# Optimization experiments

Measured on AMD Instinct MI355X. Metric: run time of the kernel, lower is better.

Reference implementation:

```python
import jax, jax.numpy as jnp
import numpy as np

B, N_AIM, N_DET, C = 4, 2048, 2048, 256  # inplanes=256, inter_channels=128


def _lin(x, w, b):
    # torch nn.Linear: y = x @ W^T + b, weight shape [out, in]
    return jnp.einsum('bnc,dc->bnd', x, w) + b


def setup_inputs() -> dict:
    key = jax.random.key(0)
    ks = jax.random.split(key, 16)
    s = 1.0 / np.sqrt(C)
    inp = {
        'detect': jax.random.normal(ks[0], (B, N_DET, C), jnp.float32),
        'aim': jax.random.normal(ks[1], (B, N_AIM, C), jnp.float32),
    }
    names = ['g', 'g2', 'theta', 'phi', 'W', 'Q']
    for i, nm in enumerate(names):
        inp[nm + '_w'] = jax.random.uniform(ks[2 + 2 * i], (C, C), jnp.float32, -s, s)
        inp[nm + '_b'] = jax.random.uniform(ks[3 + 2 * i], (C,), jnp.float32, -s, s)
    return inp


def reference(detect, aim, g_w, g_b, g2_w, g2_b, theta_w, theta_b, phi_w, phi_b, W_w, W_b, Q_w, Q_b):
    b, na, c = aim.shape
    nd = detect.shape[1]
    ic = c // 2  # inter_channels

    # view(B, ic, -1) on a contiguous [B, N, C] tensor -> row-major reshape to [B, ic, 2N]
    d_x = _lin(detect, g_w, g_b).reshape(b, ic, -1).transpose(0, 2, 1)      # (B, 2Nd, ic)
    a_x = _lin(aim, g2_w, g2_b).reshape(b, ic, -1).transpose(0, 2, 1)       # (B, 2Na, ic)
    theta_x = _lin(aim, theta_w, theta_b).reshape(b, ic, -1).transpose(0, 2, 1)  # (B, 2Na, ic)
    phi_x = _lin(detect, phi_w, phi_b).reshape(b, ic, -1)                   # (B, ic, 2Nd)

    f = jnp.matmul(theta_x, phi_x)                 # (B, 2Na, 2Nd)
    f_div_C = f / f.shape[-1]                      # scale by 2*Nd
    fi_div_C = jnp.swapaxes(f, 1, 2) / f.shape[-2] # (B, 2Nd, 2Na), scale by 2*Na

    non_aim = jnp.matmul(f_div_C, d_x)             # (B, 2Na, ic)
    non_aim = non_aim.transpose(0, 2, 1).reshape(b, na, c)
    non_aim = _lin(non_aim, W_w, W_b) + aim

    non_det = jnp.matmul(fi_div_C, a_x)            # (B, 2Nd, ic)
    non_det = non_det.transpose(0, 2, 1).reshape(b, nd, c)
    non_det = _lin(non_det, Q_w, Q_b) + detect

    return (non_det, non_aim)
```

## Files before the change

kernel.cpp:

```cpp
#include <hip/hip_runtime.h>


typedef __attribute__((ext_vector_type(4))) float  f32x4;
typedef __attribute__((ext_vector_type(8))) __bf16 bf16x8;
typedef __attribute__((ext_vector_type(8))) unsigned short u16x8;
typedef __attribute__((ext_vector_type(4))) unsigned short u16x4;

__device__ inline unsigned short f2bf(float f) {
    union { float f; unsigned u; } c; c.f = f;
    unsigned r = c.u + 0x7FFF + ((c.u >> 16) & 1);
    return (unsigned short)(r >> 16);
}
__device__ inline bf16x8 ldfrag(const unsigned short* p) {
    return __builtin_bit_cast(bf16x8, *(const u16x8*)p);
}

__global__ __launch_bounds__(256)
void lin4_kernel(const float* __restrict__ aim, const float* __restrict__ detect,
                 const float* __restrict__ w_th, const float* __restrict__ b_th,
                 const float* __restrict__ w_g2, const float* __restrict__ b_g2,
                 const float* __restrict__ w_ph, const float* __restrict__ b_ph,
                 const float* __restrict__ w_g,  const float* __restrict__ b_g,
                 unsigned short* __restrict__ T,  unsigned short* __restrict__ Ga,
                 unsigned short* __restrict__ P,  unsigned short* __restrict__ Gd)
{
    const int z = blockIdx.z, set = blockIdx.x;
    const float* A  = z ? detect : aim;
    const float* Wm = z ? (set ? w_g : w_ph) : (set ? w_g2 : w_th);
    const float* Bv = z ? (set ? b_g : b_ph) : (set ? b_g2 : b_th);
    unsigned short* O = z ? (set ? Gd : P) : (set ? Ga : T);
    const int m0 = blockIdx.y * 64;

    __shared__ unsigned short As[64][40];
    __shared__ unsigned short Bs[256][40];

    const int tid = threadIdx.x, lane = tid & 63, w = tid >> 6;
    const int wr = w >> 1, wc = w & 1, q = lane >> 4, ln = lane & 15;

    f32x4 acc[2][8] = {};

    for (int k0 = 0; k0 < 256; k0 += 32) {
        #pragma unroll
        for (int i = 0; i < 2; ++i) {
            int c = tid + i * 256, row = c >> 3, c4 = c & 7;
            float4 v = *((const float4*)(A + (size_t)(m0 + row) * 256 + k0) + c4);
            u16x4 p; p[0]=f2bf(v.x); p[1]=f2bf(v.y); p[2]=f2bf(v.z); p[3]=f2bf(v.w);
            *(u16x4*)&As[row][c4 * 4] = p;
        }
        #pragma unroll
        for (int i = 0; i < 8; ++i) {
            int c = tid + i * 256, row = c >> 3, c4 = c & 7;
            float4 v = *((const float4*)(Wm + (size_t)row * 256 + k0) + c4);
            u16x4 p; p[0]=f2bf(v.x); p[1]=f2bf(v.y); p[2]=f2bf(v.z); p[3]=f2bf(v.w);
            *(u16x4*)&Bs[row][c4 * 4] = p;
        }
        __syncthreads();
        bf16x8 af[2], bb[8];
        #pragma unroll
        for (int i = 0; i < 2; ++i) af[i] = ldfrag(&As[wr * 32 + i * 16 + ln][q * 8]);
        #pragma unroll
        for (int j = 0; j < 8; ++j) bb[j] = ldfrag(&Bs[wc * 128 + j * 16 + ln][q * 8]);
        #pragma unroll
        for (int i = 0; i < 2; ++i)
            #pragma unroll
            for (int j = 0; j < 8; ++j)
                acc[i][j] = __builtin_amdgcn_mfma_f32_16x16x32_bf16(af[i], bb[j], acc[i][j], 0, 0, 0);
        __syncthreads();
    }

    #pragma unroll
    for (int i = 0; i < 2; ++i)
        #pragma unroll
        for (int j = 0; j < 8; ++j) {
            int n = wc * 128 + j * 16 + ln;
            float bias = Bv[n];
            #pragma unroll
            for (int r = 0; r < 4; ++r) {
                int m = m0 + wr * 32 + i * 16 + q * 4 + r;
                O[(size_t)m * 256 + n] = f2bf(acc[i][j][r] + bias);
            }
        }
}

__global__ __launch_bounds__(256)
void s_part_kernel(const unsigned short* __restrict__ Gd, const unsigned short* __restrict__ P,
                   const unsigned short* __restrict__ Ga, const unsigned short* __restrict__ T,
                   float* __restrict__ Spart)
{
    const int bz = blockIdx.x;
    const int which = bz >> 7, rem = bz & 127, batch = rem >> 5, chunk = rem & 31;
    const unsigned short* A = (which ? Ga : Gd) + (size_t)batch * 524288;
    const unsigned short* B = (which ? T  : P ) + (size_t)batch * 524288;
    float* out = Spart + ((size_t)(which * 4 + batch) * 32 + chunk) * 16384;
    const int kbeg = chunk * 128;

    __shared__ unsigned short As[128][72], Bs[128][72];
    const int tid = threadIdx.x, lane = tid & 63, w = tid >> 6;
    const int wr = w >> 1, wc = w & 1, q = lane >> 4, ln = lane & 15;

    f32x4 acc[4][4] = {};

    for (int kk = 0; kk < 2; ++kk) {
        const int k0 = kbeg + kk * 64;
        #pragma unroll
        for (int i = 0; i < 4; ++i) {
            int c = tid + i * 256, row = c >> 3, c8 = c & 7;
            *(u16x8*)&As[row][c8 * 8] = *(const u16x8*)(A + (size_t)row * 4096 + k0 + c8 * 8);
            *(u16x8*)&Bs[row][c8 * 8] = *(const u16x8*)(B + (size_t)row * 4096 + k0 + c8 * 8);
        }
        __syncthreads();
        #pragma unroll
        for (int ks = 0; ks < 2; ++ks) {
            bf16x8 af[4], bb[4];
            #pragma unroll
            for (int i = 0; i < 4; ++i) af[i] = ldfrag(&As[wr * 64 + i * 16 + ln][ks * 32 + q * 8]);
            #pragma unroll
            for (int j = 0; j < 4; ++j) bb[j] = ldfrag(&Bs[wc * 64 + j * 16 + ln][ks * 32 + q * 8]);
            #pragma unroll
            for (int i = 0; i < 4; ++i)
                #pragma unroll
                for (int j = 0; j < 4; ++j)
                    acc[i][j] = __builtin_amdgcn_mfma_f32_16x16x32_bf16(af[i], bb[j], acc[i][j], 0, 0, 0);
        }
        __syncthreads();
    }

    #pragma unroll
    for (int i = 0; i < 4; ++i)
        #pragma unroll
        for (int j = 0; j < 4; ++j)
            #pragma unroll
            for (int r = 0; r < 4; ++r) {
                int m = wr * 64 + i * 16 + q * 4 + r, n = wc * 64 + j * 16 + ln;
                out[m * 128 + n] = acc[i][j][r];
            }
}

__global__ __launch_bounds__(256)
void sred_kernel(const float* __restrict__ Spart, float* __restrict__ S)
{
    const int idx = blockIdx.x * 256 + threadIdx.x;
    const int c = idx >> 14, e = idx & 16383;
    float s = 0.f;
    #pragma unroll
    for (int k = 0; k < 32; ++k) s += Spart[((size_t)(c * 32 + k) << 14) + e];
    S[idx] = s;
}

__global__ __launch_bounds__(256)
void nand_kernel(const float* __restrict__ S,
                 const unsigned short* __restrict__ T, const unsigned short* __restrict__ P,
                 unsigned short* __restrict__ NA, unsigned short* __restrict__ ND)
{
    const int which = blockIdx.z >> 2, batch = blockIdx.z & 3;
    const float* Sm = S + (size_t)(which * 4 + batch) * 16384;
    const unsigned short* Bsrc = (which ? P : T) + (size_t)batch * 524288;
    unsigned short* O = (which ? ND : NA) + (size_t)batch * 524288;
    const int j0 = blockIdx.x * 64;

    __shared__ unsigned short As[128][136];
    __shared__ unsigned short Bs[64][136];

    const int tid = threadIdx.x, lane = tid & 63, w = tid >> 6;
    const int wr = w >> 1, wc = w & 1, q = lane >> 4, ln = lane & 15;

    #pragma unroll
    for (int i = 0; i < 16; ++i) {
        int c = tid + i * 256, row = c >> 5, c4 = c & 31;
        float4 v = *((const float4*)(Sm + (size_t)row * 128) + c4);
        u16x4 p; p[0]=f2bf(v.x); p[1]=f2bf(v.y); p[2]=f2bf(v.z); p[3]=f2bf(v.w);
        *(u16x4*)&As[row][c4 * 4] = p;
    }
    #pragma unroll
    for (int i = 0; i < 4; ++i) {
        int c = tid + i * 256, k = c >> 3, jj0 = (c & 7) * 8;
        u16x8 v = *(const u16x8*)(Bsrc + (size_t)k * 4096 + j0 + jj0);
        #pragma unroll
        for (int jj = 0; jj < 8; ++jj) Bs[jj0 + jj][k] = v[jj];
    }
    __syncthreads();

    f32x4 acc[4][2] = {};
    #pragma unroll
    for (int ks = 0; ks < 4; ++ks) {
        bf16x8 af[4], bb[2];
        #pragma unroll
        for (int i = 0; i < 4; ++i) af[i] = ldfrag(&As[wr * 64 + i * 16 + ln][ks * 32 + q * 8]);
        #pragma unroll
        for (int j = 0; j < 2; ++j) bb[j] = ldfrag(&Bs[wc * 32 + j * 16 + ln][ks * 32 + q * 8]);
        #pragma unroll
        for (int i = 0; i < 4; ++i)
            #pragma unroll
            for (int j = 0; j < 2; ++j)
                acc[i][j] = __builtin_amdgcn_mfma_f32_16x16x32_bf16(af[i], bb[j], acc[i][j], 0, 0, 0);
    }

    #pragma unroll
    for (int i = 0; i < 4; ++i)
        #pragma unroll
        for (int j = 0; j < 2; ++j)
            #pragma unroll
            for (int r = 0; r < 4; ++r) {
                int m = wr * 64 + i * 16 + q * 4 + r;
                int jj = j0 + wc * 32 + j * 16 + ln;
                O[(size_t)m * 4096 + jj] = f2bf(acc[i][j][r] * (1.0f / 4096.0f));
            }
}

__global__ __launch_bounds__(256)
void final_kernel(const unsigned short* __restrict__ NA, const unsigned short* __restrict__ ND,
                  const float* __restrict__ W_w, const float* __restrict__ W_b,
                  const float* __restrict__ Q_w, const float* __restrict__ Q_b,
                  const float* __restrict__ aim, const float* __restrict__ detect,
                  float* __restrict__ out_aim, float* __restrict__ out_det)
{
    const int z = blockIdx.z;
    const unsigned short* A = z ? ND : NA;
    const float* Wm = z ? Q_w : W_w;
    const float* Bv = z ? Q_b : W_b;
    const float* R  = z ? detect : aim;
    float* O = z ? out_det : out_aim;
    const int m0 = blockIdx.y * 64, n0 = blockIdx.x * 128;

    __shared__ unsigned short As[64][40], Bs[128][40];
    const int tid = threadIdx.x, lane = tid & 63, w = tid >> 6;
    const int wr = w >> 1, wc = w & 1, q = lane >> 4, ln = lane & 15;

    f32x4 acc[2][4] = {};

    for (int k0 = 0; k0 < 256; k0 += 32) {
        {
            int row = tid >> 2, c8 = tid & 3;
            *(u16x8*)&As[row][c8 * 8] = *(const u16x8*)(A + (size_t)(m0 + row) * 256 + k0 + c8 * 8);
        }
        #pragma unroll
        for (int i = 0; i < 4; ++i) {
            int c = tid + i * 256, row = c >> 3, c4 = c & 7;
            float4 v = *((const float4*)(Wm + (size_t)(n0 + row) * 256 + k0) + c4);
            u16x4 p; p[0]=f2bf(v.x); p[1]=f2bf(v.y); p[2]=f2bf(v.z); p[3]=f2bf(v.w);
            *(u16x4*)&Bs[row][c4 * 4] = p;
        }
        __syncthreads();
        bf16x8 af[2], bb[4];
        #pragma unroll
        for (int i = 0; i < 2; ++i) af[i] = ldfrag(&As[wr * 32 + i * 16 + ln][q * 8]);
        #pragma unroll
        for (int j = 0; j < 4; ++j) bb[j] = ldfrag(&Bs[wc * 64 + j * 16 + ln][q * 8]);
        #pragma unroll
        for (int i = 0; i < 2; ++i)
            #pragma unroll
            for (int j = 0; j < 4; ++j)
                acc[i][j] = __builtin_amdgcn_mfma_f32_16x16x32_bf16(af[i], bb[j], acc[i][j], 0, 0, 0);
        __syncthreads();
    }

    #pragma unroll
    for (int i = 0; i < 2; ++i)
        #pragma unroll
        for (int j = 0; j < 4; ++j) {
            int n = n0 + wc * 64 + j * 16 + ln;
            float bias = Bv[n];
            #pragma unroll
            for (int r = 0; r < 4; ++r) {
                int m = m0 + wr * 32 + i * 16 + q * 4 + r;
                O[(size_t)m * 256 + n] = acc[i][j][r] + bias + R[(size_t)m * 256 + n];
            }
        }
}

extern "C" void kernel_launch(void* const* d_in, const int* in_sizes, int n_in,
                              void* d_out, int out_size, void* d_ws, size_t ws_size,
                              hipStream_t stream)
{
    const float* detect = (const float*)d_in[0];
    const float* aim    = (const float*)d_in[1];
    const float* g_w  = (const float*)d_in[2];  const float* g_b  = (const float*)d_in[3];
    const float* g2_w = (const float*)d_in[4];  const float* g2_b = (const float*)d_in[5];
    const float* th_w = (const float*)d_in[6];  const float* th_b = (const float*)d_in[7];
    const float* ph_w = (const float*)d_in[8];  const float* ph_b = (const float*)d_in[9];
    const float* W_w  = (const float*)d_in[10]; const float* W_b  = (const float*)d_in[11];
    const float* Q_w  = (const float*)d_in[12]; const float* Q_b  = (const float*)d_in[13];

    const size_t TOT = 8192L * 256;

    unsigned short* ws16 = (unsigned short*)d_ws;
    unsigned short* T  = ws16;
    unsigned short* P  = T  + TOT;
    unsigned short* Gd = P  + TOT;
    unsigned short* Ga = Gd + TOT;
    unsigned short* NA = Ga + TOT;
    unsigned short* ND = NA + TOT;
    float* S     = (float*)(ND + TOT);
    float* Spart = S + 2 * 4 * 16384;

    float* out_det = (float*)d_out;
    float* out_aim = out_det + TOT;

    lin4_kernel<<<dim3(2, 128, 2), 256, 0, stream>>>(
        aim, detect, th_w, th_b, g2_w, g2_b, ph_w, ph_b, g_w, g_b, T, Ga, P, Gd);
    s_part_kernel<<<dim3(256), 256, 0, stream>>>(Gd, P, Ga, T, Spart);
    sred_kernel<<<dim3(512), 256, 0, stream>>>(Spart, S);
    nand_kernel<<<dim3(64, 1, 8), 256, 0, stream>>>(S, T, P, NA, ND);
    final_kernel<<<dim3(2, 128, 2), 256, 0, stream>>>(
        NA, ND, W_w, W_b, Q_w, Q_b, aim, detect, out_aim, out_det);
}
```

Measured before the change: 148.3 us.

## Fuse S reduction via atomics and merge nand with final projection

Replaces the partial-S buffer plus separate reduction kernel with float atomicAdd into a zeroed S. It also fuses the S·X product with the W/Q output projection into one kernel that keeps the intermediate tile in shared memory. The W/Q weights are pre-converted to bf16 inside the S kernel. This removes two launches and the NA/ND and Spart global round trips. In exchange it adds a memset, atomic contention on S, nondeterministic summation order, and lower per-block parallelism in the fused kernel.

```diff
diff --git a/kernel.cpp b/kernel.cpp
--- a/kernel.cpp
+++ b/kernel.cpp
@@ -15,20 +15,24 @@
     return __builtin_bit_cast(bf16x8, *(const u16x8*)p);
 }
 
+struct Params {
+    const float *detect, *aim;
+    const float *g_w, *g2_w, *th_w, *ph_w, *W_w, *Q_w;
+    const float *g_b, *g2_b, *th_b, *ph_b, *W_b, *Q_b;
+    unsigned short *Wbf;
+    unsigned short *T, *P, *Gd, *Ga;
+    float *S;
+    float *out_det, *out_aim;
+};
+
 __global__ __launch_bounds__(256)
-void lin4_kernel(const float* __restrict__ aim, const float* __restrict__ detect,
-                 const float* __restrict__ w_th, const float* __restrict__ b_th,
-                 const float* __restrict__ w_g2, const float* __restrict__ b_g2,
-                 const float* __restrict__ w_ph, const float* __restrict__ b_ph,
-                 const float* __restrict__ w_g,  const float* __restrict__ b_g,
-                 unsigned short* __restrict__ T,  unsigned short* __restrict__ Ga,
-                 unsigned short* __restrict__ P,  unsigned short* __restrict__ Gd)
+void linall_kernel(Params p)
 {
     const int z = blockIdx.z, set = blockIdx.x;
-    const float* A  = z ? detect : aim;
-    const float* Wm = z ? (set ? w_g : w_ph) : (set ? w_g2 : w_th);
-    const float* Bv = z ? (set ? b_g : b_ph) : (set ? b_g2 : b_th);
-    unsigned short* O = z ? (set ? Gd : P) : (set ? Ga : T);
+    const float* A  = z ? p.detect : p.aim;
+    const float* Wm = z ? (set ? p.g_w : p.ph_w) : (set ? p.g2_w : p.th_w);
+    const float* Bv = z ? (set ? p.g_b : p.ph_b) : (set ? p.g2_b : p.th_b);
+    unsigned short* O = z ? (set ? p.Gd : p.P) : (set ? p.Ga : p.T);
     const int m0 = blockIdx.y * 64;
 
     __shared__ unsigned short As[64][40];
@@ -44,15 +48,15 @@
         for (int i = 0; i < 2; ++i) {
             int c = tid + i * 256, row = c >> 3, c4 = c & 7;
             float4 v = *((const float4*)(A + (size_t)(m0 + row) * 256 + k0) + c4);
-            u16x4 p; p[0]=f2bf(v.x); p[1]=f2bf(v.y); p[2]=f2bf(v.z); p[3]=f2bf(v.w);
-            *(u16x4*)&As[row][c4 * 4] = p;
+            u16x4 pk; pk[0]=f2bf(v.x); pk[1]=f2bf(v.y); pk[2]=f2bf(v.z); pk[3]=f2bf(v.w);
+            *(u16x4*)&As[row][c4 * 4] = pk;
         }
         #pragma unroll
         for (int i = 0; i < 8; ++i) {
             int c = tid + i * 256, row = c >> 3, c4 = c & 7;
             float4 v = *((const float4*)(Wm + (size_t)row * 256 + k0) + c4);
-            u16x4 p; p[0]=f2bf(v.x); p[1]=f2bf(v.y); p[2]=f2bf(v.z); p[3]=f2bf(v.w);
-            *(u16x4*)&Bs[row][c4 * 4] = p;
+            u16x4 pk; pk[0]=f2bf(v.x); pk[1]=f2bf(v.y); pk[2]=f2bf(v.z); pk[3]=f2bf(v.w);
+            *(u16x4*)&Bs[row][c4 * 4] = pk;
         }
         __syncthreads();
         bf16x8 af[2], bb[8];
@@ -83,19 +87,27 @@
 }
 
 __global__ __launch_bounds__(256)
-void s_part_kernel(const unsigned short* __restrict__ Gd, const unsigned short* __restrict__ P,
-                   const unsigned short* __restrict__ Ga, const unsigned short* __restrict__ T,
-                   float* __restrict__ Spart)
-{
-    const int bz = blockIdx.x;
-    const int which = bz >> 7, rem = bz & 127, batch = rem >> 5, chunk = rem & 31;
-    const unsigned short* A = (which ? Ga : Gd) + (size_t)batch * 524288;
-    const unsigned short* B = (which ? T  : P ) + (size_t)batch * 524288;
-    float* out = Spart + ((size_t)(which * 4 + batch) * 32 + chunk) * 16384;
+void s_atomic_kernel(Params p)
+{
+    const int bx = blockIdx.x, tid = threadIdx.x;
+
+    if (tid < 128) {
+        int fi = bx * 128 + tid;
+        const float* src = fi < 16384 ? p.W_w : p.Q_w;
+        int li = fi & 16383;
+        float4 v = ((const float4*)src)[li];
+        u16x4 pk; pk[0]=f2bf(v.x); pk[1]=f2bf(v.y); pk[2]=f2bf(v.z); pk[3]=f2bf(v.w);
+        ((u16x4*)p.Wbf)[fi] = pk;
+    }
+
+    const int which = bx >> 7, rem = bx & 127, batch = rem >> 5, chunk = rem & 31;
+    const unsigned short* A = (which ? p.Ga : p.Gd) + (size_t)batch * 524288;
+    const unsigned short* B = (which ? p.T  : p.P ) + (size_t)batch * 524288;
+    float* Sout = p.S + (size_t)(which * 4 + batch) * 16384;
     const int kbeg = chunk * 128;
 
     __shared__ unsigned short As[128][72], Bs[128][72];
-    const int tid = threadIdx.x, lane = tid & 63, w = tid >> 6;
+    const int lane = tid & 63, w = tid >> 6;
     const int wr = w >> 1, wc = w & 1, q = lane >> 4, ln = lane & 15;
 
     f32x4 acc[4][4] = {};
@@ -132,175 +144,128 @@
             #pragma unroll
             for (int r = 0; r < 4; ++r) {
                 int m = wr * 64 + i * 16 + q * 4 + r, n = wc * 64 + j * 16 + ln;
-                out[m * 128 + n] = acc[i][j][r];
+                atomicAdd(&Sout[m * 128 + n], acc[i][j][r]);
             }
 }
 
 __global__ __launch_bounds__(256)
-void sred_kernel(const float* __restrict__ Spart, float* __restrict__ S)
-{
-    const int idx = blockIdx.x * 256 + threadIdx.x;
-    const int c = idx >> 14, e = idx & 16383;
-    float s = 0.f;
-    #pragma unroll
-    for (int k = 0; k < 32; ++k) s += Spart[((size_t)(c * 32 + k) << 14) + e];
-    S[idx] = s;
-}
-
-__global__ __launch_bounds__(256)
-void nand_kernel(const float* __restrict__ S,
-                 const unsigned short* __restrict__ T, const unsigned short* __restrict__ P,
-                 unsigned short* __restrict__ NA, unsigned short* __restrict__ ND)
-{
-    const int which = blockIdx.z >> 2, batch = blockIdx.z & 3;
-    const float* Sm = S + (size_t)(which * 4 + batch) * 16384;
-    const unsigned short* Bsrc = (which ? P : T) + (size_t)batch * 524288;
-    unsigned short* O = (which ? ND : NA) + (size_t)batch * 524288;
-    const int j0 = blockIdx.x * 64;
-
-    __shared__ unsigned short As[128][136];
-    __shared__ unsigned short Bs[64][136];
-
-    const int tid = threadIdx.x, lane = tid & 63, w = tid >> 6;
+void outfused_kernel(Params p)
+{
+    const int bx = blockIdx.x, tid = threadIdx.x;
+    const int lane = tid & 63, w = tid >> 6;
     const int wr = w >> 1, wc = w & 1, q = lane >> 4, ln = lane & 15;
 
-    #pragma unroll
-    for (int i = 0; i < 16; ++i) {
-        int c = tid + i * 256, row = c >> 5, c4 = c & 31;
-        float4 v = *((const float4*)(Sm + (size_t)row * 128) + c4);
-        u16x4 p; p[0]=f2bf(v.x); p[1]=f2bf(v.y); p[2]=f2bf(v.z); p[3]=f2bf(v.w);
-        *(u16x4*)&As[row][c4 * 4] = p;
-    }
-    #pragma unroll
-    for (int i = 0; i < 4; ++i) {
-        int c = tid + i * 256, k = c >> 3, jj0 = (c & 7) * 8;
-        u16x8 v = *(const u16x8*)(Bsrc + (size_t)k * 4096 + j0 + jj0);
-        #pragma unroll
-        for (int jj = 0; jj < 8; ++jj) Bs[jj0 + jj][k] = v[jj];
-    }
+    const int which = bx >> 8, batch = (bx >> 6) & 3, s = (bx >> 2) & 15, mq = bx & 3;
+    const int m0 = mq * 32;
+    const float* Sm = p.S + (size_t)(which * 4 + batch) * 16384;
+    const unsigned short* X = (which ? p.P : p.T) + (size_t)batch * 524288;
+    const unsigned short* Wm = p.Wbf + (which ? 65536 : 0);
+    const float* Bv = which ? p.Q_b : p.W_b;
+    const float* R  = which ? p.detect : p.aim;
+    float* O = which ? p.out_det : p.out_aim;
+
+    __shared__ union {
+        struct { unsigned short Ss[32][40];  unsigned short Xs[256][40]; } g1;
+        struct { unsigned short NAs[32][264]; unsigned short Ws[256][40]; } g2;
+    } sm;
+
+    f32x4 acc1[8] = {};
+    for (int kc = 0; kc < 4; ++kc) {
+        const int k0 = kc * 32;
+        {
+            int row = tid >> 3, c4 = tid & 7;
+            float4 v = *((const float4*)(Sm + (size_t)(m0 + row) * 128 + k0) + c4);
+            u16x4 pk; pk[0]=f2bf(v.x); pk[1]=f2bf(v.y); pk[2]=f2bf(v.z); pk[3]=f2bf(v.w);
+            *(u16x4*)&sm.g1.Ss[row][c4 * 4] = pk;
+        }
+        #pragma unroll
+        for (int i = 0; i < 4; ++i) {
+            int c = tid + i * 256, k = c >> 5, j8 = (c & 31) * 8;
+            u16x8 v = *(const u16x8*)(X + (size_t)(k0 + k) * 4096 + s * 256 + j8);
+            #pragma unroll
+            for (int jj = 0; jj < 8; ++jj) sm.g1.Xs[j8 + jj][k] = v[jj];
+        }
+        __syncthreads();
+        bf16x8 af = ldfrag(&sm.g1.Ss[wr * 16 + ln][q * 8]);
+        #pragma unroll
+        for (int nt = 0; nt < 8; ++nt) {
+            bf16x8 bb = ldfrag(&sm.g1.Xs[wc * 128 + nt * 16 + ln][q * 8]);
+            acc1[nt] = __builtin_amdgcn_mfma_f32_16x16x32_bf16(af, bb, acc1[nt], 0, 0, 0);
+        }
+        __syncthreads();
+    }
+
+    #pragma unroll
+    for (int nt = 0; nt < 8; ++nt)
+        #pragma unroll
+        for (int r = 0; r < 4; ++r) {
+            int mi = wr * 16 + q * 4 + r;
+            int jj = wc * 128 + nt * 16 + ln;
+            sm.g2.NAs[mi][jj] = f2bf(acc1[nt][r] * (1.0f / 4096.0f));
+        }
     __syncthreads();
 
-    f32x4 acc[4][2] = {};
-    #pragma unroll
-    for (int ks = 0; ks < 4; ++ks) {
-        bf16x8 af[4], bb[2];
-        #pragma unroll
-        for (int i = 0; i < 4; ++i) af[i] = ldfrag(&As[wr * 64 + i * 16 + ln][ks * 32 + q * 8]);
-        #pragma unroll
-        for (int j = 0; j < 2; ++j) bb[j] = ldfrag(&Bs[wc * 32 + j * 16 + ln][ks * 32 + q * 8]);
-        #pragma unroll
-        for (int i = 0; i < 4; ++i)
-            #pragma unroll
-            for (int j = 0; j < 2; ++j)
-                acc[i][j] = __builtin_amdgcn_mfma_f32_16x16x32_bf16(af[i], bb[j], acc[i][j], 0, 0, 0);
-    }
-
-    #pragma unroll
-    for (int i = 0; i < 4; ++i)
-        #pragma unroll
-        for (int j = 0; j < 2; ++j)
-            #pragma unroll
-            for (int r = 0; r < 4; ++r) {
-                int m = wr * 64 + i * 16 + q * 4 + r;
-                int jj = j0 + wc * 32 + j * 16 + ln;
-                O[(size_t)m * 4096 + jj] = f2bf(acc[i][j][r] * (1.0f / 4096.0f));
-            }
-}
-
-__global__ __launch_bounds__(256)
-void final_kernel(const unsigned short* __restrict__ NA, const unsigned short* __restrict__ ND,
-                  const float* __restrict__ W_w, const float* __restrict__ W_b,
-                  const float* __restrict__ Q_w, const float* __restrict__ Q_b,
-                  const float* __restrict__ aim, const float* __restrict__ detect,
-                  float* __restrict__ out_aim, float* __restrict__ out_det)
-{
-    const int z = blockIdx.z;
-    const unsigned short* A = z ? ND : NA;
-    const float* Wm = z ? Q_w : W_w;
-    const float* Bv = z ? Q_b : W_b;
-    const float* R  = z ? detect : aim;
-    float* O = z ? out_det : out_aim;
-    const int m0 = blockIdx.y * 64, n0 = blockIdx.x * 128;
-
-    __shared__ unsigned short As[64][40], Bs[128][40];
-    const int tid = threadIdx.x, lane = tid & 63, w = tid >> 6;
-    const int wr = w >> 1, wc = w & 1, q = lane >> 4, ln = lane & 15;
-
-    f32x4 acc[2][4] = {};
-
-    for (int k0 = 0; k0 < 256; k0 += 32) {
-        {
-            int row = tid >> 2, c8 = tid & 3;
-            *(u16x8*)&As[row][c8 * 8] = *(const u16x8*)(A + (size_t)(m0 + row) * 256 + k0 + c8 * 8);
-        }
+    f32x4 acc2[8] = {};
+    for (int cc = 0; cc < 8; ++cc) {
+        const int c0 = cc * 32;
         #pragma unroll
         for (int i = 0; i < 4; ++i) {
-            int c = tid + i * 256, row = c >> 3, c4 = c & 7;
-            float4 v = *((const float4*)(Wm + (size_t)(n0 + row) * 256 + k0) + c4);
-            u16x4 p; p[0]=f2bf(v.x); p[1]=f2bf(v.y); p[2]=f2bf(v.z); p[3]=f2bf(v.w);
-            *(u16x4*)&Bs[row][c4 * 4] = p;
-        }
-        __syncthreads();
-        bf16x8 af[2], bb[4];
-        #pragma unroll
-        for (int i = 0; i < 2; ++i) af[i] = ldfrag(&As[wr * 32 + i * 16 + ln][q * 8]);
-        #pragma unroll
-        for (int j = 0; j < 4; ++j) bb[j] = ldfrag(&Bs[wc * 64 + j * 16 + ln][q * 8]);
-        #pragma unroll
-        for (int i = 0; i < 2; ++i)
-            #pragma unroll
-            for (int j = 0; j < 4; ++j)
-                acc[i][j] = __builtin_amdgcn_mfma_f32_16x16x32_bf16(af[i], bb[j], acc[i][j], 0, 0, 0);
-        __syncthreads();
-    }
-
-    #pragma unroll
-    for (int i = 0; i < 2; ++i)
-        #pragma unroll
-        for (int j = 0; j < 4; ++j) {
-            int n = n0 + wc * 64 + j * 16 + ln;
-            float bias = Bv[n];
-            #pragma unroll
-            for (int r = 0; r < 4; ++r) {
-                int m = m0 + wr * 32 + i * 16 + q * 4 + r;
-                O[(size_t)m * 256 + n] = acc[i][j][r] + bias + R[(size_t)m * 256 + n];
-            }
-        }
+            int c = tid + i * 256, row = c >> 2, c8 = c & 3;
+            *(u16x8*)&sm.g2.Ws[row][c8 * 8] = *(const u16x8*)(Wm + (size_t)row * 256 + c0 + c8 * 8);
+        }
+        __syncthreads();
+        bf16x8 af = ldfrag(&sm.g2.NAs[wr * 16 + ln][c0 + q * 8]);
+        #pragma unroll
+        for (int nt = 0; nt < 8; ++nt) {
+            bf16x8 bb = ldfrag(&sm.g2.Ws[wc * 128 + nt * 16 + ln][q * 8]);
+            acc2[nt] = __builtin_amdgcn_mfma_f32_16x16x32_bf16(af, bb, acc2[nt], 0, 0, 0);
+        }
+        __syncthreads();
+    }
+
+    #pragma unroll
+    for (int nt = 0; nt < 8; ++nt) {
+        int n = wc * 128 + nt * 16 + ln;
+        float bias = Bv[n];
+        #pragma unroll
+        for (int r = 0; r < 4; ++r) {
+            int mi = wr * 16 + q * 4 + r;
+            int row = (m0 + mi) * 16 + s;
+            size_t idx = ((size_t)batch * 2048 + row) * 256 + n;
+            O[idx] = acc2[nt][r] + bias + R[idx];
+        }
+    }
 }
 
 extern "C" void kernel_launch(void* const* d_in, const int* in_sizes, int n_in,
                               void* d_out, int out_size, void* d_ws, size_t ws_size,
                               hipStream_t stream)
 {
-    const float* detect = (const float*)d_in[0];
-    const float* aim    = (const float*)d_in[1];
-    const float* g_w  = (const float*)d_in[2];  const float* g_b  = (const float*)d_in[3];
-    const float* g2_w = (const float*)d_in[4];  const float* g2_b = (const float*)d_in[5];
-    const float* th_w = (const float*)d_in[6];  const float* th_b = (const float*)d_in[7];
-    const float* ph_w = (const float*)d_in[8];  const float* ph_b = (const float*)d_in[9];
-    const float* W_w  = (const float*)d_in[10]; const float* W_b  = (const float*)d_in[11];
-    const float* Q_w  = (const float*)d_in[12]; const float* Q_b  = (const float*)d_in[13];
+    Params p;
+    p.detect = (const float*)d_in[0];
+    p.aim    = (const float*)d_in[1];
+    p.g_w  = (const float*)d_in[2];  p.g_b  = (const float*)d_in[3];
+    p.g2_w = (const float*)d_in[4];  p.g2_b = (const float*)d_in[5];
+    p.th_w = (const float*)d_in[6];  p.th_b = (const float*)d_in[7];
+    p.ph_w = (const float*)d_in[8];  p.ph_b = (const float*)d_in[9];
+    p.W_w  = (const float*)d_in[10]; p.W_b  = (const float*)d_in[11];
+    p.Q_w  = (const float*)d_in[12]; p.Q_b  = (const float*)d_in[13];
 
     const size_t TOT = 8192L * 256;
 
     unsigned short* ws16 = (unsigned short*)d_ws;
-    unsigned short* T  = ws16;
-    unsigned short* P  = T  + TOT;
-    unsigned short* Gd = P  + TOT;
-    unsigned short* Ga = Gd + TOT;
-    unsigned short* NA = Ga + TOT;
-    unsigned short* ND = NA + TOT;
-    float* S     = (float*)(ND + TOT);
-    float* Spart = S + 2 * 4 * 16384;
-
-    float* out_det = (float*)d_out;
-    float* out_aim = out_det + TOT;
-
-    lin4_kernel<<<dim3(2, 128, 2), 256, 0, stream>>>(
-        aim, detect, th_w, th_b, g2_w, g2_b, ph_w, ph_b, g_w, g_b, T, Ga, P, Gd);
-    s_part_kernel<<<dim3(256), 256, 0, stream>>>(Gd, P, Ga, T, Spart);
-    sred_kernel<<<dim3(512), 256, 0, stream>>>(Spart, S);
-    nand_kernel<<<dim3(64, 1, 8), 256, 0, stream>>>(S, T, P, NA, ND);
-    final_kernel<<<dim3(2, 128, 2), 256, 0, stream>>>(
-        NA, ND, W_w, W_b, Q_w, Q_b, aim, detect, out_aim, out_det);
-}
+    p.Wbf = ws16;
+    p.T   = p.Wbf + 2 * 65536;
+    p.P   = p.T  + TOT;
+    p.Gd  = p.P  + TOT;
+    p.Ga  = p.Gd + TOT;
+    p.S   = (float*)(p.Ga + TOT);
+
+    p.out_det = (float*)d_out;
+    p.out_aim = p.out_det + TOT;
+
+    hipMemsetAsync(p.S, 0, 2 * 4 * 16384 * sizeof(float), stream);
+    linall_kernel<<<dim3(2, 128, 2), 256, 0, stream>>>(p);
+    s_atomic_kernel<<<dim3(256), 256, 0, stream>>>(p);
+    outfused_kernel<<<dim3(512), 256, 0, stream>>>(p);
+}
```

Measured after the change: 179.4 us. 1.21x slower.
